# Kernel optimization log

Measured on AMD Instinct MI355X. Metric: run time of the kernel, lower is better.

Reference implementation:

```python
import jax, jax.numpy as jnp
import numpy as np

N_ATOMS = 100000
N_EDGES = 800000
ATOM_FDIM = 133
HIDDEN = 256
DEPTH = 3
NUM_MOLS = 4096
BN_EPS = 1e-5


def setup_inputs() -> dict:
    key = jax.random.key(0)
    ks = jax.random.split(key, 16)
    f_atoms = jax.random.normal(ks[0], (N_ATOMS, ATOM_FDIM), dtype=jnp.float32)
    edge_index = jax.random.randint(ks[1], (2, N_EDGES), 0, N_ATOMS, dtype=jnp.int64)
    segment_ids = jnp.sort(jax.random.randint(ks[2], (N_ATOMS,), 0, NUM_MOLS, dtype=jnp.int64))
    s = 1.0 / np.sqrt(HIDDEN)
    return {
        "f_atoms": f_atoms,
        "W_in_w": jax.random.normal(ks[3], (ATOM_FDIM, HIDDEN), dtype=jnp.float32) / np.sqrt(ATOM_FDIM),
        "W_in_b": jnp.zeros((HIDDEN,), dtype=jnp.float32),
        "w1": jax.random.normal(ks[4], (DEPTH, HIDDEN, HIDDEN), dtype=jnp.float32) * s,
        "b1": jnp.zeros((DEPTH, HIDDEN), dtype=jnp.float32),
        "g1": jnp.ones((DEPTH, HIDDEN), dtype=jnp.float32),
        "be1": jnp.zeros((DEPTH, HIDDEN), dtype=jnp.float32),
        "w2": jax.random.normal(ks[5], (DEPTH, HIDDEN, HIDDEN), dtype=jnp.float32) * s,
        "b2": jnp.zeros((DEPTH, HIDDEN), dtype=jnp.float32),
        "g2": jnp.ones((DEPTH, HIDDEN), dtype=jnp.float32),
        "be2": jnp.zeros((DEPTH, HIDDEN), dtype=jnp.float32),
        "eps": jnp.zeros((DEPTH,), dtype=jnp.float32),
        "edge_index": edge_index,
        "segment_ids": segment_ids,
    }


def batchnorm(h, gamma, beta):
    # BatchNorm1d with batch statistics over the node dimension (training-mode math)
    mean = jnp.mean(h, axis=0)
    var = jnp.var(h, axis=0)
    return (h - mean) * jax.lax.rsqrt(var + BN_EPS) * gamma + beta


def reference(f_atoms, W_in_w, W_in_b, w1, b1, g1, be1, w2, b2, g2, be2, eps,
              edge_index, segment_ids):
    src, dst = edge_index[0], edge_index[1]
    x = jax.nn.relu(f_atoms @ W_in_w + W_in_b)  # [N, H]
    for i in range(DEPTH):
        agg = jnp.zeros_like(x).at[dst].add(x[src])  # gather + scatter-add
        h = agg + (1.0 + eps[i]) * x                 # epsilon self-term
        h = jax.nn.relu(batchnorm(h @ w1[i] + b1[i], g1[i], be1[i]))
        h = jax.nn.relu(batchnorm(h @ w2[i] + b2[i], g2[i], be2[i]))
        x = h  # dropout = identity (eval)
    sums = jax.ops.segment_sum(x, segment_ids, num_segments=NUM_MOLS)
    counts = jax.ops.segment_sum(jnp.ones((x.shape[0],), x.dtype), segment_ids,
                                 num_segments=NUM_MOLS)
    return sums / jnp.maximum(counts, 1.0)[:, None]  # per-molecule mean
```

## Files before the change

### kernel.cpp

```cpp
#include <hip/hip_runtime.h>
#include <hip/hip_bf16.h>

#define NA 100000
#define NE 800000
#define FDIM 133
#define KIN 192
#define H 256
#define NMOL 4096

typedef __attribute__((ext_vector_type(8))) short s16x8;
typedef __attribute__((ext_vector_type(4))) float f32x4;

__device__ __forceinline__ float bf2f(unsigned short h) {
    unsigned u = ((unsigned)h) << 16;
    return __builtin_bit_cast(float, u);
}
__device__ __forceinline__ unsigned short f2bf(float f) {
    unsigned u = __builtin_bit_cast(unsigned, f);
    u = u + 0x7FFFu + ((u >> 16) & 1u);
    return (unsigned short)(u >> 16);
}

__device__ __forceinline__ int swz(int row, int g) {
    return row * 64 + ((g ^ (row & 7)) << 3);
}

template<bool A_F32, bool AFFINE, bool RELU_OUT, bool STATS>
__global__ __launch_bounds__(512, 4) void gemm_k(
    const void* __restrict__ Avoid,
    const unsigned short* __restrict__ BT,
    const float* __restrict__ bias,
    const float* __restrict__ aSc, const float* __restrict__ aSh,
    unsigned short* __restrict__ C,
    float* __restrict__ stSum, float* __restrict__ stSq,
    int M, int Kpad)
{
    __shared__ short lsAB[(128 + 256) * 64];
    __shared__ float lsSc[256], lsSh[256];
    __shared__ float lsS[256], lsQ[256];
    short* lsA = lsAB;
    short* lsB = lsAB + 128 * 64;

    const int t = threadIdx.x;
    const int m0 = blockIdx.x * 128;

    if (STATS && t < 256) { lsS[t] = 0.f; lsQ[t] = 0.f; }
    if (AFFINE && t < 256) { lsSc[t] = aSc[t]; lsSh[t] = aSh[t]; }
    if (AFFINE) __syncthreads();

    const int lane = t & 63;
    const int wid = t >> 6;
    const int wm = wid >> 2, wn = wid & 3;
    const int fr = lane & 15, fg = lane >> 4;
    const int srow = t >> 3;
    const int sg = t & 7;

    f32x4 acc[4][4];
    #pragma unroll
    for (int i = 0; i < 4; i++)
        #pragma unroll
        for (int j = 0; j < 4; j++)
            acc[i][j] = f32x4{0.f, 0.f, 0.f, 0.f};

    const int nK = Kpad >> 6;
    s16x8 ra[2], rb[4];

    auto loadRegs = [&](int kc) {
        const int k0 = kc * 64;
        #pragma unroll
        for (int p = 0; p < 2; ++p) {
            int r = srow + p * 64;
            int ga = m0 + r;
            if (A_F32) {
                const float* Af = (const float*)Avoid;
                s16x8 v;
                #pragma unroll
                for (int e = 0; e < 8; ++e) {
                    int k = k0 + sg * 8 + e;
                    float f = (ga < M && k < FDIM) ? Af[(size_t)ga * FDIM + k] : 0.f;
                    v[e] = (short)f2bf(f);
                }
                ra[p] = v;
            } else {
                const unsigned short* A = (const unsigned short*)Avoid;
                s16x8 z = {0,0,0,0,0,0,0,0};
                ra[p] = (ga < M) ? *(const s16x8*)(A + (size_t)ga * Kpad + k0 + sg * 8) : z;
            }
        }
        #pragma unroll
        for (int p = 0; p < 4; ++p)
            rb[p] = *(const s16x8*)(BT + (size_t)(srow + p * 64) * Kpad + k0 + sg * 8);
    };
    auto writeLds = [&](int kc) {
        const int k0 = kc * 64;
        #pragma unroll
        for (int p = 0; p < 2; ++p) {
            s16x8 va = ra[p];
            if (AFFINE) {
                #pragma unroll
                for (int e = 0; e < 8; ++e) {
                    int k = k0 + sg * 8 + e;
                    float f = bf2f((unsigned short)va[e]);
                    f = fmaxf(f * lsSc[k] + lsSh[k], 0.f);
                    va[e] = (short)f2bf(f);
                }
            }
            *(s16x8*)&lsA[swz(srow + p * 64, sg)] = va;
        }
        #pragma unroll
        for (int p = 0; p < 4; ++p)
            *(s16x8*)&lsB[swz(srow + p * 64, sg)] = rb[p];
    };

    loadRegs(0);
    for (int kc = 0; kc < nK; ++kc) {
        writeLds(kc);
        __syncthreads();
        if (kc + 1 < nK) loadRegs(kc + 1);
        #pragma unroll
        for (int ks = 0; ks < 2; ++ks) {
            s16x8 af[4], bg[4];
            #pragma unroll
            for (int mi = 0; mi < 4; ++mi)
                af[mi] = *(const s16x8*)&lsA[swz(wm * 64 + mi * 16 + fr, ks * 4 + fg)];
            #pragma unroll
            for (int ni = 0; ni < 4; ++ni)
                bg[ni] = *(const s16x8*)&lsB[swz(wn * 64 + ni * 16 + fr, ks * 4 + fg)];
            #pragma unroll
            for (int mi = 0; mi < 4; ++mi)
                #pragma unroll
                for (int ni = 0; ni < 4; ++ni)
                    acc[mi][ni] = __builtin_amdgcn_mfma_f32_16x16x32_bf16(
                        af[mi], bg[ni], acc[mi][ni], 0, 0, 0);
        }
        __syncthreads();
    }

    const int CST = 264;
    #pragma unroll
    for (int hm = 0; hm < 2; ++hm) {
        __syncthreads();
        if (wm == hm) {
            #pragma unroll
            for (int ni = 0; ni < 4; ++ni) {
                int lcol = wn * 64 + ni * 16 + fr;
                float bc = bias[lcol];
                float cs = 0.f, cq = 0.f;
                #pragma unroll
                for (int mi = 0; mi < 4; ++mi) {
                    #pragma unroll
                    for (int r = 0; r < 4; ++r) {
                        int rl = mi * 16 + fg * 4 + r;
                        float v = acc[mi][ni][r] + bc;
                        if (RELU_OUT) v = fmaxf(v, 0.f);
                        if (STATS && (m0 + hm * 64 + rl < M)) { cs += v; cq += v * v; }
                        lsAB[rl * CST + lcol] = (short)f2bf(v);
                    }
                }
                if (STATS) {
                    atomicAdd(&lsS[lcol], cs);
                    atomicAdd(&lsQ[lcol], cq);
                }
            }
        }
        __syncthreads();
        #pragma unroll
        for (int p = 0; p < 4; ++p) {
            int idx = p * 512 + t;
            int rl = idx >> 5;
            int col = (idx & 31) * 8;
            int row = m0 + hm * 64 + rl;
            if (row < M)
                *(s16x8*)(C + (size_t)row * H + col) = *(const s16x8*)&lsAB[rl * CST + col];
        }
    }

    if (STATS) {
        __syncthreads();
        if (t < 256) {
            atomicAdd(&stSum[t], lsS[t]);
            atomicAdd(&stSq[t], lsQ[t]);
        }
    }
}

__global__ void bnfin_k(float* __restrict__ sum, float* __restrict__ sumsq,
                        const float* __restrict__ g, const float* __restrict__ be,
                        float* __restrict__ scOut, float* __restrict__ shOut) {
    int c = threadIdx.x;
    float mean = sum[c] * (1.0f / NA);
    float var = sumsq[c] * (1.0f / NA) - mean * mean;
    float sc = g[c] * rsqrtf(var + 1e-5f);
    scOut[c] = sc;
    shOut[c] = be[c] - mean * sc;
    sum[c] = 0.f; sumsq[c] = 0.f;
}

__global__ void zero_k(int* __restrict__ counts, float* __restrict__ st, int* __restrict__ rowstart) {
    int i = blockIdx.x * 256 + threadIdx.x;
    if (i < NA) counts[i] = 0;
    if (blockIdx.x == 0) {
        st[threadIdx.x] = 0.f; st[threadIdx.x + 256] = 0.f;
        if (threadIdx.x == 0) rowstart[NA] = NE;
    }
}

__global__ void hist_k(const int* __restrict__ dst, int* __restrict__ counts) {
    int e = blockIdx.x * 256 + threadIdx.x;
    if (e < NE) atomicAdd(&counts[dst[e]], 1);
}
__global__ void scan1_k(const int* __restrict__ counts, int* __restrict__ excl, int* __restrict__ bsum) {
    __shared__ int sd[256];
    int i = blockIdx.x * 256 + threadIdx.x;
    int c = (i < NA) ? counts[i] : 0;
    sd[threadIdx.x] = c;
    __syncthreads();
    for (int off = 1; off < 256; off <<= 1) {
        int v = (threadIdx.x >= off) ? sd[threadIdx.x - off] : 0;
        __syncthreads();
        sd[threadIdx.x] += v;
        __syncthreads();
    }
    if (i < NA) excl[i] = sd[threadIdx.x] - c;
    if (threadIdx.x == 255) bsum[blockIdx.x] = sd[255];
}
__global__ void scan2_k(int* __restrict__ bsum, int nb) {
    __shared__ int sd[512];
    int t = threadIdx.x;
    int v = (t < nb) ? bsum[t] : 0;
    sd[t] = v;
    __syncthreads();
    for (int off = 1; off < 512; off <<= 1) {
        int u = (t >= off) ? sd[t - off] : 0;
        __syncthreads();
        sd[t] += u;
        __syncthreads();
    }
    if (t < nb) bsum[t] = sd[t] - v;
}
__global__ void scan3_k(int* __restrict__ rowstart, const int* __restrict__ bsum, int* __restrict__ cursor) {
    int i = blockIdx.x * 256 + threadIdx.x;
    if (i < NA) {
        int v = rowstart[i] + bsum[blockIdx.x];
        rowstart[i] = v;
        cursor[i] = v;
    }
}
__global__ void fill_k(const int* __restrict__ src, const int* __restrict__ dstArr,
                       int* __restrict__ cursor, int* __restrict__ esrc) {
    int e = blockIdx.x * 256 + threadIdx.x;
    if (e < NE) {
        int d = dstArr[e];
        int pos = atomicAdd(&cursor[d], 1);
        esrc[pos] = src[e];
    }
}

template<bool AFF>
__global__ __launch_bounds__(256) void agg_k(const unsigned short* __restrict__ X,
    const float* __restrict__ sc, const float* __restrict__ sh,
    const int* __restrict__ rowstart,
    const int* __restrict__ esrc, const float* __restrict__ epsArr, int layer,
    unsigned short* __restrict__ AGG)
{
    int wid = threadIdx.x >> 6, lane = threadIdx.x & 63;
    int row = blockIdx.x * 4 + wid;
    int half = lane >> 5;
    int c0 = (lane & 31) * 8;

    float s8[8], h8[8];
    if (AFF) {
        f32x4 a = *(const f32x4*)(sc + c0), b = *(const f32x4*)(sc + c0 + 4);
        f32x4 c = *(const f32x4*)(sh + c0), d = *(const f32x4*)(sh + c0 + 4);
        #pragma unroll
        for (int e = 0; e < 4; e++) { s8[e] = a[e]; s8[e + 4] = b[e]; h8[e] = c[e]; h8[e + 4] = d[e]; }
    }

    float a0[8] = {0,0,0,0,0,0,0,0}, a1[8] = {0,0,0,0,0,0,0,0};
    auto addv = [&](s16x8 u, float* a) {
        #pragma unroll
        for (int e = 0; e < 8; e++) {
            float f = bf2f((unsigned short)u[e]);
            if (AFF) f = fmaxf(f * s8[e] + h8[e], 0.f);
            a[e] += f;
        }
    };

    int s = rowstart[row], eEnd = rowstart[row + 1];
    int cnt = eEnd - s, mid = s + (cnt >> 1);
    int i = half ? mid : s;
    int end = half ? eEnd : mid;
    for (; i + 3 < end; i += 4) {
        int e0 = esrc[i], e1 = esrc[i + 1], e2 = esrc[i + 2], e3 = esrc[i + 3];
        s16x8 u0 = *(const s16x8*)(X + (size_t)e0 * H + c0);
        s16x8 u1 = *(const s16x8*)(X + (size_t)e1 * H + c0);
        s16x8 u2 = *(const s16x8*)(X + (size_t)e2 * H + c0);
        s16x8 u3 = *(const s16x8*)(X + (size_t)e3 * H + c0);
        addv(u0, a0); addv(u1, a1); addv(u2, a0); addv(u3, a1);
    }
    for (; i < end; ++i) {
        int e0 = esrc[i];
        s16x8 u = *(const s16x8*)(X + (size_t)e0 * H + c0);
        addv(u, a0);
    }

    if (half == 0) {
        float e1 = 1.0f + epsArr[layer];
        s16x8 u = *(const s16x8*)(X + (size_t)row * H + c0);
        #pragma unroll
        for (int e = 0; e < 8; e++) {
            float f = bf2f((unsigned short)u[e]);
            if (AFF) f = fmaxf(f * s8[e] + h8[e], 0.f);
            a0[e] += f * e1;
        }
    }

    s16x8 o;
    #pragma unroll
    for (int e = 0; e < 8; e++) {
        float tot = a0[e] + a1[e];
        tot += __shfl_xor(tot, 32);
        o[e] = (short)f2bf(tot);
    }
    if (half == 0)
        *(s16x8*)(AGG + (size_t)row * H + c0) = o;
}

__global__ void prep_all_k(const float* __restrict__ Win, const float* __restrict__ w1,
                           const float* __restrict__ w2, unsigned short* __restrict__ BTall) {
    int i = blockIdx.x * 256 + threadIdx.x;
    const int NIN = 256 * KIN;
    if (i < NIN) {
        int n = i / KIN, k = i % KIN;
        BTall[i] = (k < FDIM) ? f2bf(Win[(size_t)k * 256 + n]) : (unsigned short)0;
    } else if (i < NIN + 6 * 65536) {
        int j = i - NIN;
        int d = j >> 16, r = j & 65535;
        int n = r >> 8, k = r & 255;
        const float* W = (d & 1) ? w2 : w1;
        BTall[i] = f2bf(W[(size_t)(d >> 1) * 65536 + (size_t)k * 256 + n]);
    }
}

__global__ void molstart_k(const int* __restrict__ seg, int* __restrict__ ms) {
    int m = blockIdx.x * 256 + threadIdx.x;
    if (m <= NMOL) {
        int lo = 0, hi = NA;
        while (lo < hi) { int mid = (lo + hi) >> 1; if (seg[mid] < m) lo = mid + 1; else hi = mid; }
        ms[m] = lo;
    }
}
__global__ __launch_bounds__(64) void mean_k(const unsigned short* __restrict__ X,
    const float* __restrict__ sc, const float* __restrict__ sh,
    const int* __restrict__ ms, float* __restrict__ out)
{
    int m = blockIdx.x, lane = threadIdx.x;
    int half = lane >> 5;
    int c0 = (lane & 31) * 8;
    float s8[8], h8[8];
    {
        f32x4 a = *(const f32x4*)(sc + c0), b = *(const f32x4*)(sc + c0 + 4);
        f32x4 c = *(const f32x4*)(sh + c0), d = *(const f32x4*)(sh + c0 + 4);
        #pragma unroll
        for (int e = 0; e < 4; e++) { s8[e] = a[e]; s8[e + 4] = b[e]; h8[e] = c[e]; h8[e + 4] = d[e]; }
    }
    int a = ms[m], b = ms[m + 1];
    float acc[8] = {0,0,0,0,0,0,0,0};
    for (int r = a + half; r < b; r += 2) {
        s16x8 u = *(const s16x8*)(X + (size_t)r * H + c0);
        #pragma unroll
        for (int e = 0; e < 8; e++)
            acc[e] += fmaxf(bf2f((unsigned short)u[e]) * s8[e] + h8[e], 0.f);
    }
    float inv = (b > a) ? 1.0f / (float)(b - a) : 0.0f;
    f32x4 o0, o1;
    #pragma unroll
    for (int e = 0; e < 8; e++) {
        float tot = acc[e] + __shfl_xor(acc[e], 32);
        tot *= inv;
        if (e < 4) o0[e] = tot; else o1[e - 4] = tot;
    }
    if (half == 0) {
        *(f32x4*)(out + (size_t)m * H + c0) = o0;
        *(f32x4*)(out + (size_t)m * H + c0 + 4) = o1;
    }
}

extern "C" void kernel_launch(void* const* d_in, const int* in_sizes, int n_in,
                              void* d_out, int out_size, void* d_ws, size_t ws_size,
                              hipStream_t stream) {
    const float* f_atoms = (const float*)d_in[0];
    const float* W_in_w  = (const float*)d_in[1];
    const float* W_in_b  = (const float*)d_in[2];
    const float* w1  = (const float*)d_in[3];
    const float* b1  = (const float*)d_in[4];
    const float* g1  = (const float*)d_in[5];
    const float* be1 = (const float*)d_in[6];
    const float* w2  = (const float*)d_in[7];
    const float* b2  = (const float*)d_in[8];
    const float* g2  = (const float*)d_in[9];
    const float* be2 = (const float*)d_in[10];
    const float* epsArr = (const float*)d_in[11];
    const int* edge = (const int*)d_in[12];
    const int* seg  = (const int*)d_in[13];
    float* out = (float*)d_out;

    char* w = (char*)d_ws;
    size_t off = 0;
    auto alloc = [&](size_t bytes) {
        char* p = w + off;
        off = (off + bytes + 255) & ~(size_t)255;
        return p;
    };
    unsigned short* X   = (unsigned short*)alloc((size_t)NA * H * 2);
    unsigned short* AGG = (unsigned short*)alloc((size_t)NA * H * 2);
    unsigned short* T1  = (unsigned short*)alloc((size_t)NA * H * 2);
    unsigned short* BTall = (unsigned short*)alloc(((size_t)256 * KIN + 6 * 65536) * 2);
    float* stSum = (float*)alloc(256 * 4);
    float* stSq  = (float*)alloc(256 * 4);
    float* sc1 = (float*)alloc(256 * 4);
    float* sh1 = (float*)alloc(256 * 4);
    float* sc2 = (float*)alloc(256 * 4);
    float* sh2 = (float*)alloc(256 * 4);
    int* counts   = (int*)alloc((size_t)NA * 4);
    int* rowstart = (int*)alloc((size_t)(NA + 1) * 4);
    int* cursor   = (int*)alloc((size_t)NA * 4);
    int* esrc     = (int*)alloc((size_t)NE * 4);
    int* bsum     = (int*)alloc(512 * 4);
    int* ms       = (int*)alloc((NMOL + 1) * 4);

    unsigned short* BTin = BTall;
    unsigned short* BT1[3], *BT2[3];
    for (int d = 0; d < 3; ++d) {
        BT1[d] = BTall + 256 * KIN + (size_t)(2 * d) * 65536;
        BT2[d] = BTall + 256 * KIN + (size_t)(2 * d + 1) * 65536;
    }

    const int* esrcIn = edge;
    const int* edst   = edge + NE;

    zero_k<<<(NA + 255) / 256, 256, 0, stream>>>(counts, stSum, rowstart);
    prep_all_k<<<(256 * KIN + 6 * 65536 + 255) / 256, 256, 0, stream>>>(W_in_w, w1, w2, BTall);

    hist_k<<<(NE + 255) / 256, 256, 0, stream>>>(edst, counts);
    scan1_k<<<391, 256, 0, stream>>>(counts, rowstart, bsum);
    scan2_k<<<1, 512, 0, stream>>>(bsum, 391);
    scan3_k<<<391, 256, 0, stream>>>(rowstart, bsum, cursor);
    fill_k<<<(NE + 255) / 256, 256, 0, stream>>>(esrcIn, edst, cursor, esrc);
    molstart_k<<<(NMOL + 256) / 256, 256, 0, stream>>>(seg, ms);

    const int GB = (NA + 127) / 128;

    gemm_k<true, false, true, false><<<GB, 512, 0, stream>>>(
        f_atoms, BTin, W_in_b, nullptr, nullptr, X, nullptr, nullptr, NA, KIN);

    for (int d = 0; d < 3; ++d) {
        if (d == 0)
            agg_k<false><<<NA / 4, 256, 0, stream>>>(X, nullptr, nullptr,
                rowstart, esrc, epsArr, d, AGG);
        else
            agg_k<true><<<NA / 4, 256, 0, stream>>>(X, sc2, sh2,
                rowstart, esrc, epsArr, d, AGG);
        gemm_k<false, false, false, true><<<GB, 512, 0, stream>>>(
            AGG, BT1[d], b1 + d * 256, nullptr, nullptr, T1, stSum, stSq, NA, 256);
        bnfin_k<<<1, 256, 0, stream>>>(stSum, stSq, g1 + d * 256, be1 + d * 256, sc1, sh1);
        gemm_k<false, true, false, true><<<GB, 512, 0, stream>>>(
            T1, BT2[d], b2 + d * 256, sc1, sh1, X, stSum, stSq, NA, 256);
        bnfin_k<<<1, 256, 0, stream>>>(stSum, stSq, g2 + d * 256, be2 + d * 256, sc2, sh2);
    }

    mean_k<<<NMOL, 64, 0, stream>>>(X, sc2, sh2, ms, out);
}
```

Measured before the change: 866.6 us.

## Fuse neighbor aggregation into first GEMM's A-tile load, drop AGG buffer

Replaces the separate aggregation kernel plus first per-layer GEMM with a single kernel that gathers neighbor rows (with optional BN affine+ReLU and epsilon self-term) directly while building each A tile in shared memory, then does the MFMA GEMM and BN stats. This removes the write and re-read of the AGG intermediate and one launch per layer. It also adds nontemporal loads of T1 in the second GEMM and nontemporal stores of the fused output. The fused kernel uses only 8 threads per row per k-chunk for the irregular gather, with lower occupancy (launch bounds 2), so gather latency may stall the GEMM.

```diff
diff --git a/kernel.cpp b/kernel.cpp
--- a/kernel.cpp
+++ b/kernel.cpp
@@ -10,6 +10,7 @@
 
 typedef __attribute__((ext_vector_type(8))) short s16x8;
 typedef __attribute__((ext_vector_type(4))) float f32x4;
+typedef __attribute__((ext_vector_type(4))) unsigned int u32x4;
 
 __device__ __forceinline__ float bf2f(unsigned short h) {
     unsigned u = ((unsigned)h) << 16;
@@ -20,12 +21,192 @@
     u = u + 0x7FFFu + ((u >> 16) & 1u);
     return (unsigned short)(u >> 16);
 }
+__device__ __forceinline__ void nt_store16(s16x8 v, void* p) {
+    __builtin_nontemporal_store(__builtin_bit_cast(u32x4, v), (u32x4*)p);
+}
+__device__ __forceinline__ s16x8 nt_load16(const void* p) {
+    return __builtin_bit_cast(s16x8, __builtin_nontemporal_load((const u32x4*)p));
+}
 
 __device__ __forceinline__ int swz(int row, int g) {
     return row * 64 + ((g ^ (row & 7)) << 3);
 }
 
-template<bool A_F32, bool AFFINE, bool RELU_OUT, bool STATS>
+template<bool AFF>
+__global__ __launch_bounds__(512, 2) void gemmG_k(
+    const unsigned short* __restrict__ X,
+    const unsigned short* __restrict__ BT,
+    const float* __restrict__ bias,
+    const float* __restrict__ aSc, const float* __restrict__ aSh,
+    const int* __restrict__ rowstart, const int* __restrict__ esrc,
+    const float* __restrict__ epsArr, int layer,
+    unsigned short* __restrict__ C,
+    float* __restrict__ stSum, float* __restrict__ stSq, int M)
+{
+    __shared__ short lsAB[(128 + 256) * 64];
+    __shared__ float lsSc[256], lsSh[256], lsS[256], lsQ[256];
+    short* lsA = lsAB;
+    short* lsB = lsAB + 128 * 64;
+
+    const int t = threadIdx.x;
+    const int m0 = blockIdx.x * 128;
+    if (t < 256) {
+        lsS[t] = 0.f; lsQ[t] = 0.f;
+        if (AFF) { lsSc[t] = aSc[t]; lsSh[t] = aSh[t]; }
+    }
+    if (AFF) __syncthreads();
+
+    const int lane = t & 63, wid = t >> 6;
+    const int wm = wid >> 2, wn = wid & 3;
+    const int fr = lane & 15, fg = lane >> 4;
+    const int srow = t >> 3, sg = t & 7;
+
+    const int gr0 = m0 + srow, gr1 = m0 + srow + 64;
+    int s0 = 0, e0 = 0, s1 = 0, e1 = 0;
+    if (gr0 < M) { s0 = rowstart[gr0]; e0 = rowstart[gr0 + 1]; }
+    if (gr1 < M) { s1 = rowstart[gr1]; e1 = rowstart[gr1 + 1]; }
+    const float epv = 1.0f + epsArr[layer];
+
+    f32x4 acc[4][4];
+    #pragma unroll
+    for (int i = 0; i < 4; i++)
+        #pragma unroll
+        for (int j = 0; j < 4; j++)
+            acc[i][j] = f32x4{0.f, 0.f, 0.f, 0.f};
+
+    s16x8 rb[4];
+    auto loadB = [&](int kc) {
+        #pragma unroll
+        for (int p = 0; p < 4; ++p)
+            rb[p] = *(const s16x8*)(BT + (size_t)(srow + p * 64) * 256 + kc * 64 + sg * 8);
+    };
+
+    loadB(0);
+    for (int kc = 0; kc < 4; ++kc) {
+        const int cb = kc * 64 + sg * 8;
+        float sc8[8], sh8[8];
+        if (AFF) {
+            #pragma unroll
+            for (int j = 0; j < 8; ++j) { sc8[j] = lsSc[cb + j]; sh8[j] = lsSh[cb + j]; }
+        }
+        auto gath = [&](int gr, int s, int e) -> s16x8 {
+            float a[8] = {0,0,0,0,0,0,0,0};
+            if (gr < M) {
+                float b[8] = {0,0,0,0,0,0,0,0};
+                {
+                    s16x8 u = *(const s16x8*)(X + (size_t)gr * H + cb);
+                    #pragma unroll
+                    for (int j = 0; j < 8; ++j) {
+                        float f = bf2f((unsigned short)u[j]);
+                        if (AFF) f = fmaxf(f * sc8[j] + sh8[j], 0.f);
+                        a[j] = f * epv;
+                    }
+                }
+                int i = s;
+                for (; i + 1 < e; i += 2) {
+                    int n0 = esrc[i], n1 = esrc[i + 1];
+                    s16x8 u0 = *(const s16x8*)(X + (size_t)n0 * H + cb);
+                    s16x8 u1 = *(const s16x8*)(X + (size_t)n1 * H + cb);
+                    #pragma unroll
+                    for (int j = 0; j < 8; ++j) {
+                        float f0 = bf2f((unsigned short)u0[j]);
+                        float f1 = bf2f((unsigned short)u1[j]);
+                        if (AFF) {
+                            f0 = fmaxf(f0 * sc8[j] + sh8[j], 0.f);
+                            f1 = fmaxf(f1 * sc8[j] + sh8[j], 0.f);
+                        }
+                        a[j] += f0; b[j] += f1;
+                    }
+                }
+                if (i < e) {
+                    int n0 = esrc[i];
+                    s16x8 u = *(const s16x8*)(X + (size_t)n0 * H + cb);
+                    #pragma unroll
+                    for (int j = 0; j < 8; ++j) {
+                        float f = bf2f((unsigned short)u[j]);
+                        if (AFF) f = fmaxf(f * sc8[j] + sh8[j], 0.f);
+                        a[j] += f;
+                    }
+                }
+                #pragma unroll
+                for (int j = 0; j < 8; ++j) a[j] += b[j];
+            }
+            s16x8 o;
+            #pragma unroll
+            for (int j = 0; j < 8; ++j) o[j] = (short)f2bf(a[j]);
+            return o;
+        };
+        s16x8 vA0 = gath(gr0, s0, e0);
+        s16x8 vA1 = gath(gr1, s1, e1);
+        *(s16x8*)&lsA[swz(srow, sg)] = vA0;
+        *(s16x8*)&lsA[swz(srow + 64, sg)] = vA1;
+        #pragma unroll
+        for (int p = 0; p < 4; ++p)
+            *(s16x8*)&lsB[swz(srow + p * 64, sg)] = rb[p];
+        __syncthreads();
+        if (kc < 3) loadB(kc + 1);
+        #pragma unroll
+        for (int ks = 0; ks < 2; ++ks) {
+            s16x8 af[4], bg[4];
+            #pragma unroll
+            for (int mi = 0; mi < 4; ++mi)
+                af[mi] = *(const s16x8*)&lsA[swz(wm * 64 + mi * 16 + fr, ks * 4 + fg)];
+            #pragma unroll
+            for (int ni = 0; ni < 4; ++ni)
+                bg[ni] = *(const s16x8*)&lsB[swz(wn * 64 + ni * 16 + fr, ks * 4 + fg)];
+            #pragma unroll
+            for (int mi = 0; mi < 4; ++mi)
+                #pragma unroll
+                for (int ni = 0; ni < 4; ++ni)
+                    acc[mi][ni] = __builtin_amdgcn_mfma_f32_16x16x32_bf16(
+                        af[mi], bg[ni], acc[mi][ni], 0, 0, 0);
+        }
+        __syncthreads();
+    }
+
+    const int CST = 264;
+    #pragma unroll
+    for (int hm = 0; hm < 2; ++hm) {
+        __syncthreads();
+        if (wm == hm) {
+            #pragma unroll
+            for (int ni = 0; ni < 4; ++ni) {
+                int lcol = wn * 64 + ni * 16 + fr;
+                float bc = bias[lcol];
+                float cs = 0.f, cq = 0.f;
+                #pragma unroll
+                for (int mi = 0; mi < 4; ++mi) {
+                    #pragma unroll
+                    for (int r = 0; r < 4; ++r) {
+                        int rl = mi * 16 + fg * 4 + r;
+                        float v = acc[mi][ni][r] + bc;
+                        if (m0 + hm * 64 + rl < M) { cs += v; cq += v * v; }
+                        lsAB[rl * CST + lcol] = (short)f2bf(v);
+                    }
+                }
+                atomicAdd(&lsS[lcol], cs);
+                atomicAdd(&lsQ[lcol], cq);
+            }
+        }
+        __syncthreads();
+        #pragma unroll
+        for (int p = 0; p < 4; ++p) {
+            int idx = p * 512 + t;
+            int rl = idx >> 5;
+            int col = (idx & 31) * 8;
+            int row = m0 + hm * 64 + rl;
+            if (row < M)
+                nt_store16(*(const s16x8*)&lsAB[rl * CST + col], C + (size_t)row * H + col);
+        }
+    }
+    __syncthreads();
+    if (t < 256) {
+        atomicAdd(&stSum[t], lsS[t]);
+        atomicAdd(&stSq[t], lsQ[t]);
+    }
+}
+
+template<bool A_F32, bool AFFINE, bool RELU_OUT, bool STATS, bool NTA>
 __global__ __launch_bounds__(512, 4) void gemm_k(
     const void* __restrict__ Avoid,
     const unsigned short* __restrict__ BT,
@@ -84,7 +265,8 @@
             } else {
                 const unsigned short* A = (const unsigned short*)Avoid;
                 s16x8 z = {0,0,0,0,0,0,0,0};
-                ra[p] = (ga < M) ? *(const s16x8*)(A + (size_t)ga * Kpad + k0 + sg * 8) : z;
+                const void* ap = A + (size_t)ga * Kpad + k0 + sg * 8;
+                ra[p] = (ga < M) ? (NTA ? nt_load16(ap) : *(const s16x8*)ap) : z;
             }
         }
         #pragma unroll
@@ -254,76 +436,6 @@
         int pos = atomicAdd(&cursor[d], 1);
         esrc[pos] = src[e];
     }
-}
-
-template<bool AFF>
-__global__ __launch_bounds__(256) void agg_k(const unsigned short* __restrict__ X,
-    const float* __restrict__ sc, const float* __restrict__ sh,
-    const int* __restrict__ rowstart,
-    const int* __restrict__ esrc, const float* __restrict__ epsArr, int layer,
-    unsigned short* __restrict__ AGG)
-{
-    int wid = threadIdx.x >> 6, lane = threadIdx.x & 63;
-    int row = blockIdx.x * 4 + wid;
-    int half = lane >> 5;
-    int c0 = (lane & 31) * 8;
-
-    float s8[8], h8[8];
-    if (AFF) {
-        f32x4 a = *(const f32x4*)(sc + c0), b = *(const f32x4*)(sc + c0 + 4);
-        f32x4 c = *(const f32x4*)(sh + c0), d = *(const f32x4*)(sh + c0 + 4);
-        #pragma unroll
-        for (int e = 0; e < 4; e++) { s8[e] = a[e]; s8[e + 4] = b[e]; h8[e] = c[e]; h8[e + 4] = d[e]; }
-    }
-
-    float a0[8] = {0,0,0,0,0,0,0,0}, a1[8] = {0,0,0,0,0,0,0,0};
-    auto addv = [&](s16x8 u, float* a) {
-        #pragma unroll
-        for (int e = 0; e < 8; e++) {
-            float f = bf2f((unsigned short)u[e]);
-            if (AFF) f = fmaxf(f * s8[e] + h8[e], 0.f);
-            a[e] += f;
-        }
-    };
-
-    int s = rowstart[row], eEnd = rowstart[row + 1];
-    int cnt = eEnd - s, mid = s + (cnt >> 1);
-    int i = half ? mid : s;
-    int end = half ? eEnd : mid;
-    for (; i + 3 < end; i += 4) {
-        int e0 = esrc[i], e1 = esrc[i + 1], e2 = esrc[i + 2], e3 = esrc[i + 3];
-        s16x8 u0 = *(const s16x8*)(X + (size_t)e0 * H + c0);
-        s16x8 u1 = *(const s16x8*)(X + (size_t)e1 * H + c0);
-        s16x8 u2 = *(const s16x8*)(X + (size_t)e2 * H + c0);
-        s16x8 u3 = *(const s16x8*)(X + (size_t)e3 * H + c0);
-        addv(u0, a0); addv(u1, a1); addv(u2, a0); addv(u3, a1);
-    }
-    for (; i < end; ++i) {
-        int e0 = esrc[i];
-        s16x8 u = *(const s16x8*)(X + (size_t)e0 * H + c0);
-        addv(u, a0);
-    }
-
-    if (half == 0) {
-        float e1 = 1.0f + epsArr[layer];
-        s16x8 u = *(const s16x8*)(X + (size_t)row * H + c0);
-        #pragma unroll
-        for (int e = 0; e < 8; e++) {
-            float f = bf2f((unsigned short)u[e]);
-            if (AFF) f = fmaxf(f * s8[e] + h8[e], 0.f);
-            a0[e] += f * e1;
-        }
-    }
-
-    s16x8 o;
-    #pragma unroll
-    for (int e = 0; e < 8; e++) {
-        float tot = a0[e] + a1[e];
-        tot += __shfl_xor(tot, 32);
-        o[e] = (short)f2bf(tot);
-    }
-    if (half == 0)
-        *(s16x8*)(AGG + (size_t)row * H + c0) = o;
 }
 
 __global__ void prep_all_k(const float* __restrict__ Win, const float* __restrict__ w1,
@@ -413,7 +525,6 @@
         return p;
     };
     unsigned short* X   = (unsigned short*)alloc((size_t)NA * H * 2);
-    unsigned short* AGG = (unsigned short*)alloc((size_t)NA * H * 2);
     unsigned short* T1  = (unsigned short*)alloc((size_t)NA * H * 2);
     unsigned short* BTall = (unsigned short*)alloc(((size_t)256 * KIN + 6 * 65536) * 2);
     float* stSum = (float*)alloc(256 * 4);
@@ -451,20 +562,18 @@
 
     const int GB = (NA + 127) / 128;
 
-    gemm_k<true, false, true, false><<<GB, 512, 0, stream>>>(
+    gemm_k<true, false, true, false, false><<<GB, 512, 0, stream>>>(
         f_atoms, BTin, W_in_b, nullptr, nullptr, X, nullptr, nullptr, NA, KIN);
 
     for (int d = 0; d < 3; ++d) {
         if (d == 0)
-            agg_k<false><<<NA / 4, 256, 0, stream>>>(X, nullptr, nullptr,
-                rowstart, esrc, epsArr, d, AGG);
+            gemmG_k<false><<<GB, 512, 0, stream>>>(X, BT1[d], b1 + d * 256,
+                nullptr, nullptr, rowstart, esrc, epsArr, d, T1, stSum, stSq, NA);
         else
-            agg_k<true><<<NA / 4, 256, 0, stream>>>(X, sc2, sh2,
-                rowstart, esrc, epsArr, d, AGG);
-        gemm_k<false, false, false, true><<<GB, 512, 0, stream>>>(
-            AGG, BT1[d], b1 + d * 256, nullptr, nullptr, T1, stSum, stSq, NA, 256);
+            gemmG_k<true><<<GB, 512, 0, stream>>>(X, BT1[d], b1 + d * 256,
+                sc2, sh2, rowstart, esrc, epsArr, d, T1, stSum, stSq, NA);
         bnfin_k<<<1, 256, 0, stream>>>(stSum, stSq, g1 + d * 256, be1 + d * 256, sc1, sh1);
-        gemm_k<false, true, false, true><<<GB, 512, 0, stream>>>(
+        gemm_k<false, true, false, true, true><<<GB, 512, 0, stream>>>(
             T1, BT2[d], b2 + d * 256, sc1, sh1, X, stSum, stSq, NA, 256);
         bnfin_k<<<1, 256, 0, stream>>>(stSum, stSq, g2 + d * 256, be2 + d * 256, sc2, sh2);
     }
```

Result: slower. 1.161 ms (+34.0%).
